# Kernel tuning notes

Hardware: AMD Instinct MI355X
Metric: run time of the kernel (lower is better)

The kernel has to match this reference:

```python
import jax, jax.numpy as jnp
import numpy as np

STRIDE = 32
ANCHORS = np.array([[10, 13], [16, 30], [33, 23], [30, 61], [62, 45],
                    [59, 119], [116, 90], [156, 198], [373, 326]], np.float32)
ALL_ANCH = ANCHORS / STRIDE           # [9,2] anchor w,h in grid units
ANCH_MASK = [6, 7, 8]
MASKED_ANCH = ALL_ANCH[ANCH_MASK]     # [3,2]
N_CLASSES = 80
N_ANCHORS = 3
IGNORE_THRE = 0.5


def _bce_sum(p, t, w=1.0):
    # torch BCELoss(sum): clamps log terms at -100 to avoid 0*inf
    lp = jnp.maximum(jnp.log(p), -100.0)
    lq = jnp.maximum(jnp.log(1.0 - p), -100.0)
    return jnp.sum(-w * (t * lp + (1.0 - t) * lq))


def _iou_xywh(a, b):
    # a: [B,N,4], b: [B,K,4] in (cx,cy,w,h) -> IoU [B,N,K]
    tl = jnp.maximum(a[:, :, None, :2] - a[:, :, None, 2:] / 2,
                     b[:, None, :, :2] - b[:, None, :, 2:] / 2)
    br = jnp.minimum(a[:, :, None, :2] + a[:, :, None, 2:] / 2,
                     b[:, None, :, :2] + b[:, None, :, 2:] / 2)
    en = jnp.all(tl < br, axis=-1).astype(a.dtype)
    inter = jnp.prod(br - tl, axis=-1) * en
    area_a = a[:, :, 2] * a[:, :, 3]
    area_b = b[:, :, 2] * b[:, :, 3]
    return inter / (area_a[:, :, None] + area_b[:, None, :] - inter)


def setup_inputs() -> dict:
    key = jax.random.key(0)
    k1, k2, k3, k4 = jax.random.split(key, 4)
    B, M, F, A, NC = 128, 60, 19, 3, 80
    output = jax.random.normal(k1, (B, A * (5 + NC), F, F), jnp.float32)
    cxy = jax.random.uniform(k2, (B, M, 2), jnp.float32, 100.0, 500.0)
    wh = jax.random.uniform(k3, (B, M, 2), jnp.float32, 64.0, 192.0)
    cls = jax.random.randint(k4, (B, M, 1), 0, NC).astype(jnp.float32)
    labels = jnp.concatenate([cxy - wh / 2, cxy + wh / 2, cls], axis=-1)
    return {"output": output, "labels": labels}


def reference(output, labels):
    B = output.shape[0]
    F = output.shape[2]
    n_ch = 5 + N_CLASSES
    labels = jax.lax.stop_gradient(labels)  # torch detaches labels

    # [B, A, F, F, n_ch]; sigmoid on x,y,obj,cls; raw on w,h
    out = output.reshape(B, N_ANCHORS, n_ch, F, F).transpose(0, 1, 3, 4, 2)
    out = jnp.concatenate([jax.nn.sigmoid(out[..., :2]), out[..., 2:4],
                           jax.nn.sigmoid(out[..., 4:])], axis=-1)

    # decoded pred boxes (grid units), detached as in torch (.data)
    xs = jnp.arange(F, dtype=out.dtype)
    wa = jnp.asarray(MASKED_ANCH[:, 0])[None, :, None, None]
    ha = jnp.asarray(MASKED_ANCH[:, 1])[None, :, None, None]
    px = out[..., 0] + xs[None, None, None, :]
    py = out[..., 1] + xs[None, None, :, None]
    pw = jnp.exp(out[..., 2]) * wa
    ph = jnp.exp(out[..., 3]) * ha
    pred = jax.lax.stop_gradient(jnp.stack([px, py, pw, ph], axis=-1))

    valid = labels.sum(axis=2) > 0                               # [B,M]
    tx = jnp.floor(labels[..., 0] / STRIDE)
    ty = jnp.floor(labels[..., 1] / STRIDE)
    tw = jnp.floor((labels[..., 2] - labels[..., 0]) / STRIDE)
    th = jnp.floor((labels[..., 3] - labels[..., 1]) / STRIDE)
    ti = tx.astype(jnp.int32)
    tj = ty.astype(jnp.int32)

    # anchor matching: IoU of (0,0,w,h) truths vs (0,0,aw,ah) ref anchors
    ref_wh = jnp.asarray(ALL_ANCH)                               # [9,2]
    mw = jnp.minimum(tw[..., None], ref_wh[:, 0])
    mh = jnp.minimum(th[..., None], ref_wh[:, 1])
    en = ((mw > 0) & (mh > 0)).astype(out.dtype)
    inter = mw * mh * en
    aiou = inter / (tw[..., None] * th[..., None]
                    + ref_wh[:, 0] * ref_wh[:, 1] - inter)       # [B,M,9]
    best_all = jnp.argmax(aiou, axis=-1)                         # [B,M]
    best_n = best_all % 3
    best_mask = best_all >= ANCH_MASK[0]

    # ignore mask from pred-vs-truth IoU
    truth_box = jnp.stack([tx, ty, tw, th], axis=-1)             # [B,M,4]
    ious = _iou_xywh(pred.reshape(B, -1, 4), truth_box)          # [B,AFF,M]
    ious = ious * valid[:, None, :].astype(out.dtype)
    best_iou = ious.max(axis=-1)
    obj_mask = (best_iou <= IGNORE_THRE).astype(out.dtype).reshape(B, N_ANCHORS, F, F)

    # scatter matched truths into (b, a, j, i) cells
    matched = valid & best_mask                                  # [B,M]
    NT = B * N_ANCHORS * F * F
    b_idx = jnp.broadcast_to(jnp.arange(B, dtype=jnp.int32)[:, None], matched.shape)
    flat = ((b_idx * N_ANCHORS + best_n.astype(jnp.int32)) * F + tj) * F + ti
    flat = jnp.where(matched, flat, NT).reshape(-1)              # NT is OOB -> dropped

    obj_mask = obj_mask.reshape(-1).at[flat].set(1.0, mode='drop').reshape(B, N_ANCHORS, F, F)
    tgt_mask = jnp.zeros((NT, 4 + N_CLASSES), out.dtype).at[flat].set(1.0, mode='drop')
    tgt_mask = tgt_mask.reshape(B, N_ANCHORS, F, F, 4 + N_CLASSES)

    txf = tx - tx.astype(jnp.int32).astype(out.dtype)   # exactly 0 (as in torch)
    tyf = ty - ty.astype(jnp.int32).astype(out.dtype)
    anch = jnp.asarray(MASKED_ANCH)[best_n]                      # [B,M,2]
    twt = jnp.log(tw / anch[..., 0] + 1e-16)
    tht = jnp.log(th / anch[..., 1] + 1e-16)
    onehot = jax.nn.one_hot(labels[..., 4].astype(jnp.int32), N_CLASSES, dtype=out.dtype)
    trow = jnp.concatenate([txf[..., None], tyf[..., None], twt[..., None],
                            tht[..., None], jnp.ones_like(txf)[..., None],
                            onehot], axis=-1).reshape(-1, n_ch)
    target = jnp.zeros((NT, n_ch), out.dtype).at[flat].set(trow, mode='drop')
    target = target.reshape(B, N_ANCHORS, F, F, n_ch)

    scale_val = jnp.sqrt(2.0 - tw * th / (F * F))                # [B,M]
    srow = jnp.broadcast_to(scale_val[..., None], scale_val.shape + (2,)).reshape(-1, 2)
    tgt_scale = jnp.zeros((NT, 2), out.dtype).at[flat].set(srow, mode='drop')
    tgt_scale = tgt_scale.reshape(B, N_ANCHORS, F, F, 2)

    # apply masks (in-place multiplies in torch)
    out_xy = out[..., :2] * tgt_mask[..., :2]
    out_wh = out[..., 2:4] * tgt_mask[..., 2:4] * tgt_scale
    out_obj = out[..., 4] * obj_mask
    out_cls = out[..., 5:] * tgt_mask[..., 4:]
    tgt_xy = target[..., :2] * tgt_mask[..., :2]
    tgt_wh = target[..., 2:4] * tgt_mask[..., 2:4] * tgt_scale
    tgt_obj = target[..., 4] * obj_mask
    tgt_cls = target[..., 5:] * tgt_mask[..., 4:]

    loss_xy = _bce_sum(out_xy, tgt_xy, tgt_scale * tgt_scale)
    loss_wh = 0.5 * jnp.sum((out_wh - tgt_wh) ** 2)
    loss_obj = _bce_sum(out_obj, tgt_obj)
    loss_cls = _bce_sum(out_cls, tgt_cls)
    out_full = jnp.concatenate([out_xy, out_wh, out_obj[..., None], out_cls], axis=-1)
    tgt_full = jnp.concatenate([tgt_xy, tgt_wh, tgt_obj[..., None], tgt_cls], axis=-1)
    loss_l2 = jnp.sum((out_full - tgt_full) ** 2)
    loss = loss_xy + loss_wh + loss_obj + loss_cls
    return (loss, loss_xy, loss_wh, loss_obj, loss_cls, loss_l2)
```

## Files before the change

kernel.cpp:

```cpp
#include <hip/hip_runtime.h>

#define NB 128
#define NM 60
#define NF 19
#define NA 3
#define NCELL (NF*NF)
#define NCH 85
#define NCHTOT (NA*NCH)
#define HALFC 192
#define TPB 384
#define NWAVE (TPB/64)
#define NBLK (NB*NA*2)
#define MAXLIST 64

__device__ __constant__ float c_aw[9] = {0.3125f, 0.5f, 1.03125f, 0.9375f, 1.9375f, 1.84375f, 3.625f, 4.875f, 11.65625f};
__device__ __constant__ float c_ah[9] = {0.40625f, 0.9375f, 0.71875f, 1.90625f, 1.40625f, 3.71875f, 2.8125f, 6.1875f, 10.1875f};

__device__ __forceinline__ float clog(float v) { return fmaxf(__logf(v), -100.0f); }
__device__ __forceinline__ float sigm(float x) { return 1.0f / (1.0f + __expf(-x)); }

__device__ __forceinline__ float wave_sum(float v) {
    for (int off = 32; off > 0; off >>= 1) v += __shfl_down(v, off, 64);
    return v;
}

__global__ __launch_bounds__(TPB) void k_main(const float* __restrict__ out,
                                              const float* __restrict__ labels,
                                              float* __restrict__ partial) {
    __shared__ float4 s_box[NM];
    __shared__ float  s_ar[NM];
    __shared__ float  s_scale[NM], s_twt[NM], s_tht[NM], s_txf[NM], s_tyf[NM];
    __shared__ int    s_cls[NM];
    __shared__ int    s_win[NCELL];
    __shared__ int    s_ign[HALFC];
    __shared__ int    s_list[MAXLIST];
    __shared__ int    s_n;
    __shared__ float  s_red[NWAVE][5];

    const int blk  = blockIdx.x;
    const int ba   = blk >> 1;
    const int half = blk & 1;
    const int b = ba / NA, a = ba % NA;
    const int tid = threadIdx.x;
    const int grp   = (tid >= HALFC) ? 1 : 0;
    const int local = tid - grp * HALFC;
    const int cell  = half * HALFC + local;
    const bool active = cell < NCELL;

    float x1 = 0.f, y1 = 0.f, x2 = 0.f, y2 = 0.f, cf = 0.f;
    if (tid < NM) {
        const float* l = labels + ((size_t)b * NM + tid) * 5;
        x1 = l[0]; y1 = l[1]; x2 = l[2]; y2 = l[3]; cf = l[4];
    }
    const float* obase = out + ((size_t)b * NCHTOT + a * NCH) * NCELL;
    float r0 = 0.f, r1 = 0.f, r2 = 0.f, r3 = 0.f, r4 = 0.f;
    if (active) {
        r0 = obase[0 * NCELL + cell];
        r1 = obase[1 * NCELL + cell];
        r2 = obase[2 * NCELL + cell];
        r3 = obase[3 * NCELL + cell];
        if (grp == 0) r4 = obase[4 * NCELL + cell];
    }

    for (int c = tid; c < NCELL; c += TPB) s_win[c] = -1;
    if (tid == 0) s_n = 0;
    __syncthreads();

    if (tid < NM) {
        bool valid = (x1 + y1 + x2 + y2 + cf) > 0.0f;
        float tx = floorf(x1 * 0.03125f);
        float ty = floorf(y1 * 0.03125f);
        float tw = floorf((x2 - x1) * 0.03125f);
        float th = floorf((y2 - y1) * 0.03125f);
        int ti = (int)tx, tj = (int)ty;
        float bst = -1.0f; int bi = 0;
        #pragma unroll
        for (int q = 0; q < 9; q++) {
            float mw = fminf(tw, c_aw[q]), mh = fminf(th, c_ah[q]);
            float inter = (mw > 0.0f && mh > 0.0f) ? mw * mh : 0.0f;
            float iou = inter / (tw * th + c_aw[q] * c_ah[q] - inter);
            if (iou > bst) { bst = iou; bi = q; }
        }
        int bn = bi % 3;
        s_box[tid] = valid ? make_float4(tx - 0.5f * tw, ty - 0.5f * th,
                                         tx + 0.5f * tw, ty + 0.5f * th)
                           : make_float4(3.0e8f, 3.0e8f, 3.0e8f, 3.0e8f);
        s_ar[tid]    = valid ? tw * th : 1.0e30f;
        s_scale[tid] = sqrtf(2.0f - tw * th * (1.0f / (float)NCELL));
        s_twt[tid]   = __logf(tw / c_aw[6 + bn] + 1e-16f);
        s_tht[tid]   = __logf(th / c_ah[6 + bn] + 1e-16f);
        s_txf[tid]   = tx - (float)ti;
        s_tyf[tid]   = ty - (float)tj;
        s_cls[tid]   = (int)cf;
        if (valid && bi >= 6 && bn == a &&
            ti >= 0 && ti < NF && tj >= 0 && tj < NF) {
            atomicMax(&s_win[tj * NF + ti], tid);
        }
    }
    __syncthreads();

    int ii = cell % NF, jj = cell / NF;
    float sx = sigm(r0), sy = sigm(r1), sobj = sigm(r4);
    float pw = __expf(r2) * c_aw[6 + a], ph = __expf(r3) * c_ah[6 + a];
    float px = sx + (float)ii, py = sy + (float)jj;
    float px1 = px - 0.5f * pw, px2 = px + 0.5f * pw;
    float py1 = py - 0.5f * ph, py2 = py + 0.5f * ph;
    float parea = pw * ph;

    bool ign = false;
    const int mstart = grp * (NM / 2);
    #pragma unroll 6
    for (int m = mstart; m < mstart + NM / 2; m++) {
        float4 tb = s_box[m];
        float dx = fminf(px2, tb.z) - fmaxf(px1, tb.x);
        float dy = fminf(py2, tb.w) - fmaxf(py1, tb.y);
        float inter = fmaxf(dx, 0.0f) * fmaxf(dy, 0.0f);
        ign = ign || (3.0f * inter > parea + s_ar[m]);
    }
    if (grp == 1) s_ign[local] = ign ? 1 : 0;
    __syncthreads();

    float lxy = 0.f, lwh = 0.f, lobj = 0.f, lcls = 0.f, ll2 = 0.f;
    if (grp == 0 && active) {
        ign = ign || (s_ign[local] != 0);
        int w = s_win[cell];
        if (w >= 0) {
            float s = s_scale[w], s2 = s * s;
            float txf = s_txf[w], tyf = s_tyf[w];
            float dw = r2 - s_twt[w], dh = r3 - s_tht[w];
            lxy = -s2 * (txf * clog(sx) + (1.0f - txf) * clog(1.0f - sx)
                       + tyf * clog(sy) + (1.0f - tyf) * clog(1.0f - sy));
            float whsq = s2 * (dw * dw + dh * dh);
            lwh = 0.5f * whsq;
            lobj = -clog(sobj);
            ll2 = (sx - txf) * (sx - txf) + (sy - tyf) * (sy - tyf)
                + whsq + (sobj - 1.0f) * (sobj - 1.0f);
            int pos = atomicAdd(&s_n, 1);
            if (pos < MAXLIST) s_list[pos] = cell | (s_cls[w] << 16);
        } else if (!ign) {
            lobj = -clog(1.0f - sobj);
            ll2 = sobj * sobj;
        }
    }
    __syncthreads();

    int nwork = min(s_n, MAXLIST) * 96;
    for (int w = tid; w < nwork; w += TPB) {
        int e = w / 96;
        int c = w - e * 96;
        if (c < 80) {
            int packed = s_list[e];
            int mc = packed & 0xFFFF, k = packed >> 16;
            float sc = sigm(obase[(size_t)(5 + c) * NCELL + mc]);
            bool isk = (c == k);
            lcls -= isk ? clog(sc) : clog(1.0f - sc);
            float d = isk ? (sc - 1.0f) : sc;
            ll2 += d * d;
        }
    }

    float v0 = wave_sum(lxy), v1 = wave_sum(lwh), v2 = wave_sum(lobj);
    float v3 = wave_sum(lcls), v4 = wave_sum(ll2);
    int lane = tid & 63, wid = tid >> 6;
    if (lane == 0) {
        s_red[wid][0] = v0; s_red[wid][1] = v1; s_red[wid][2] = v2;
        s_red[wid][3] = v3; s_red[wid][4] = v4;
    }
    __syncthreads();
    if (tid < 5) {
        float s = 0.0f;
        #pragma unroll
        for (int wv = 0; wv < NWAVE; wv++) s += s_red[wv][tid];
        partial[(size_t)blk * 5 + tid] = s;
    }
}

__global__ __launch_bounds__(256) void k_reduce(const float* __restrict__ partial,
                                                float* __restrict__ res) {
    __shared__ float s[4][5];
    int tid = threadIdx.x;
    float acc[5] = {0.f, 0.f, 0.f, 0.f, 0.f};
    for (int i = tid; i < NBLK; i += 256) {
        const float* p = partial + (size_t)i * 5;
        acc[0] += p[0]; acc[1] += p[1]; acc[2] += p[2];
        acc[3] += p[3]; acc[4] += p[4];
    }
    #pragma unroll
    for (int j = 0; j < 5; j++) acc[j] = wave_sum(acc[j]);
    int lane = tid & 63, wid = tid >> 6;
    if (lane == 0) {
        #pragma unroll
        for (int j = 0; j < 5; j++) s[wid][j] = acc[j];
    }
    __syncthreads();
    if (tid == 0) {
        float t[5];
        #pragma unroll
        for (int j = 0; j < 5; j++) t[j] = s[0][j] + s[1][j] + s[2][j] + s[3][j];
        res[0] = t[0] + t[1] + t[2] + t[3];
        res[1] = t[0]; res[2] = t[1]; res[3] = t[2];
        res[4] = t[3]; res[5] = t[4];
    }
}

extern "C" void kernel_launch(void* const* d_in, const int* in_sizes, int n_in,
                              void* d_out, int out_size, void* d_ws, size_t ws_size,
                              hipStream_t stream) {
    (void)in_sizes; (void)n_in; (void)out_size; (void)ws_size;
    const float* output = (const float*)d_in[0];
    const float* labels = (const float*)d_in[1];
    float* res = (float*)d_out;
    float* partial = (float*)d_ws;

    k_main<<<NBLK, TPB, 0, stream>>>(output, labels, partial);
    k_reduce<<<1, 256, 0, stream>>>(partial, res);
}
```

Baseline: 91.29 us.

## Merge half-blocks into one block per anchor and match targets via packed keys

Uses one block per (batch, anchor) with one thread per grid cell instead of two blocks that split cells and targets across thread groups. Each thread scans all targets for the ignore test and finds its assigned target by comparing a packed cell/anchor key, replacing the shared winner table, atomicMax and cross-group ignore exchange. This removes two barriers, shared-memory initialisation and atomics, but doubles the per-thread loop length and halves the number of blocks.

```diff
diff --git a/kernel.cpp b/kernel.cpp
--- a/kernel.cpp
+++ b/kernel.cpp
@@ -7,10 +7,9 @@
 #define NCELL (NF*NF)
 #define NCH 85
 #define NCHTOT (NA*NCH)
-#define HALFC 192
 #define TPB 384
 #define NWAVE (TPB/64)
-#define NBLK (NB*NA*2)
+#define NBLK (NB*NA)
 #define MAXLIST 64
 
 __device__ __constant__ float c_aw[9] = {0.3125f, 0.5f, 1.03125f, 0.9375f, 1.9375f, 1.84375f, 3.625f, 4.875f, 11.65625f};
@@ -29,22 +28,17 @@
                                               float* __restrict__ partial) {
     __shared__ float4 s_box[NM];
     __shared__ float  s_ar[NM];
+    __shared__ int    s_meta[NM];
     __shared__ float  s_scale[NM], s_twt[NM], s_tht[NM], s_txf[NM], s_tyf[NM];
     __shared__ int    s_cls[NM];
-    __shared__ int    s_win[NCELL];
-    __shared__ int    s_ign[HALFC];
     __shared__ int    s_list[MAXLIST];
     __shared__ int    s_n;
     __shared__ float  s_red[NWAVE][5];
 
-    const int blk  = blockIdx.x;
-    const int ba   = blk >> 1;
-    const int half = blk & 1;
+    const int ba  = blockIdx.x;
     const int b = ba / NA, a = ba % NA;
     const int tid = threadIdx.x;
-    const int grp   = (tid >= HALFC) ? 1 : 0;
-    const int local = tid - grp * HALFC;
-    const int cell  = half * HALFC + local;
+    const int cell = tid;
     const bool active = cell < NCELL;
 
     float x1 = 0.f, y1 = 0.f, x2 = 0.f, y2 = 0.f, cf = 0.f;
@@ -59,12 +53,9 @@
         r1 = obase[1 * NCELL + cell];
         r2 = obase[2 * NCELL + cell];
         r3 = obase[3 * NCELL + cell];
-        if (grp == 0) r4 = obase[4 * NCELL + cell];
-    }
-
-    for (int c = tid; c < NCELL; c += TPB) s_win[c] = -1;
+        r4 = obase[4 * NCELL + cell];
+    }
     if (tid == 0) s_n = 0;
-    __syncthreads();
 
     if (tid < NM) {
         bool valid = (x1 + y1 + x2 + y2 + cf) > 0.0f;
@@ -85,21 +76,22 @@
         s_box[tid] = valid ? make_float4(tx - 0.5f * tw, ty - 0.5f * th,
                                          tx + 0.5f * tw, ty + 0.5f * th)
                            : make_float4(3.0e8f, 3.0e8f, 3.0e8f, 3.0e8f);
-        s_ar[tid]    = valid ? tw * th : 1.0e30f;
+        s_ar[tid]  = valid ? tw * th : 1.0e30f;
+        bool m_ok = valid && bi >= 6 &&
+                    ti >= 0 && ti < NF && tj >= 0 && tj < NF;
+        s_meta[tid] = m_ok ? (ti | (tj << 8) | (bn << 16) | (1 << 24))
+                           : (int)0xFFFFFFFF;
         s_scale[tid] = sqrtf(2.0f - tw * th * (1.0f / (float)NCELL));
         s_twt[tid]   = __logf(tw / c_aw[6 + bn] + 1e-16f);
         s_tht[tid]   = __logf(th / c_ah[6 + bn] + 1e-16f);
         s_txf[tid]   = tx - (float)ti;
         s_tyf[tid]   = ty - (float)tj;
         s_cls[tid]   = (int)cf;
-        if (valid && bi >= 6 && bn == a &&
-            ti >= 0 && ti < NF && tj >= 0 && tj < NF) {
-            atomicMax(&s_win[tj * NF + ti], tid);
-        }
     }
     __syncthreads();
 
     int ii = cell % NF, jj = cell / NF;
+    const int mykey = ii | (jj << 8) | (a << 16) | (1 << 24);
     float sx = sigm(r0), sy = sigm(r1), sobj = sigm(r4);
     float pw = __expf(r2) * c_aw[6 + a], ph = __expf(r3) * c_ah[6 + a];
     float px = sx + (float)ii, py = sy + (float)jj;
@@ -108,22 +100,19 @@
     float parea = pw * ph;
 
     bool ign = false;
-    const int mstart = grp * (NM / 2);
+    int w = -1;
     #pragma unroll 6
-    for (int m = mstart; m < mstart + NM / 2; m++) {
+    for (int m = 0; m < NM; m++) {
         float4 tb = s_box[m];
         float dx = fminf(px2, tb.z) - fmaxf(px1, tb.x);
         float dy = fminf(py2, tb.w) - fmaxf(py1, tb.y);
         float inter = fmaxf(dx, 0.0f) * fmaxf(dy, 0.0f);
         ign = ign || (3.0f * inter > parea + s_ar[m]);
-    }
-    if (grp == 1) s_ign[local] = ign ? 1 : 0;
-    __syncthreads();
+        w = (s_meta[m] == mykey) ? m : w;
+    }
 
     float lxy = 0.f, lwh = 0.f, lobj = 0.f, lcls = 0.f, ll2 = 0.f;
-    if (grp == 0 && active) {
-        ign = ign || (s_ign[local] != 0);
-        int w = s_win[cell];
+    if (active) {
         if (w >= 0) {
             float s = s_scale[w], s2 = s * s;
             float txf = s_txf[w], tyf = s_tyf[w];
@@ -145,9 +134,9 @@
     __syncthreads();
 
     int nwork = min(s_n, MAXLIST) * 96;
-    for (int w = tid; w < nwork; w += TPB) {
-        int e = w / 96;
-        int c = w - e * 96;
+    for (int wk = tid; wk < nwork; wk += TPB) {
+        int e = wk / 96;
+        int c = wk - e * 96;
         if (c < 80) {
             int packed = s_list[e];
             int mc = packed & 0xFFFF, k = packed >> 16;
@@ -171,7 +160,7 @@
         float s = 0.0f;
         #pragma unroll
         for (int wv = 0; wv < NWAVE; wv++) s += s_red[wv][tid];
-        partial[(size_t)blk * 5 + tid] = s;
+        partial[(size_t)ba * 5 + tid] = s;
     }
 }
 
```

Result: slower. 98.50 us (+7.9%).
